# Optimization experiments

Hardware: AMD Instinct MI355X
Metric: run time of the kernel (lower is better)

The kernel has to match this reference:

```python
import jax, jax.numpy as jnp
import numpy as np

NUM_GRAPHS = 256
NEG_SLOPE = 0.2


def gat_layer(x, src, dst, W, a_src, a_dst, bias, concat):
    # x: [N, Fin], W: [Fin, H*C], a_src/a_dst: [H, C], bias: [H*C] or [C]
    N = x.shape[0]
    H, C = a_src.shape
    xl = (x @ W).reshape(N, H, C)                      # per-head projections
    e_src = jnp.sum(xl * a_src, axis=-1)               # [N, H]
    e_dst = jnp.sum(xl * a_dst, axis=-1)               # [N, H]
    e = jax.nn.leaky_relu(e_src[src] + e_dst[dst], NEG_SLOPE)  # [E, H]
    # edge softmax over variable-size neighbor sets (grouped by dst)
    m = jax.ops.segment_max(e, dst, num_segments=N)    # [N, H]
    m = jnp.where(jnp.isfinite(m), m, 0.0)
    ee = jnp.exp(e - m[dst])
    s = jax.ops.segment_sum(ee, dst, num_segments=N)   # [N, H]
    alpha = ee / (s[dst] + 1e-16)                      # [E, H]
    msg = alpha[:, :, None] * xl[src]                  # [E, H, C]
    out = jax.ops.segment_sum(msg, dst, num_segments=N)  # [N, H, C]
    out = out.reshape(N, H * C) if concat else out.mean(axis=1)
    return out + bias


def setup_inputs() -> dict:
    key = jax.random.key(0)
    ks = jax.random.split(key, 12)
    N, E, Fin, H, C, Fout = 100000, 1600000, 128, 8, 16, 64
    x = jax.random.normal(ks[0], (N, Fin), dtype=jnp.float32)
    edge_index = jax.random.randint(ks[1], (2, E), 0, N, dtype=jnp.int32)
    batch = jnp.sort(jax.random.randint(ks[2], (N,), 0, NUM_GRAPHS, dtype=jnp.int32))
    sc = 0.1
    W1 = jax.random.normal(ks[3], (Fin, H * C), dtype=jnp.float32) * sc
    att_src1 = jax.random.normal(ks[4], (H, C), dtype=jnp.float32) * sc
    att_dst1 = jax.random.normal(ks[5], (H, C), dtype=jnp.float32) * sc
    bias1 = jnp.zeros((H * C,), dtype=jnp.float32)
    W2 = jax.random.normal(ks[6], (H * C, Fout), dtype=jnp.float32) * sc
    att_src2 = jax.random.normal(ks[7], (1, Fout), dtype=jnp.float32) * sc
    att_dst2 = jax.random.normal(ks[8], (1, Fout), dtype=jnp.float32) * sc
    bias2 = jnp.zeros((Fout,), dtype=jnp.float32)
    return {"x": x, "W1": W1, "att_src1": att_src1, "att_dst1": att_dst1,
            "bias1": bias1, "W2": W2, "att_src2": att_src2, "att_dst2": att_dst2,
            "bias2": bias2, "edge_index": edge_index, "batch": batch}


def reference(x, W1, att_src1, att_dst1, bias1, W2, att_src2, att_dst2, bias2,
              edge_index, batch):
    N = x.shape[0]
    loop = jnp.arange(N, dtype=edge_index.dtype)
    src = jnp.concatenate([edge_index[0], loop])  # add self-loops (PyG default)
    dst = jnp.concatenate([edge_index[1], loop])
    # dropout is identity in eval mode
    h = gat_layer(x, src, dst, W1, att_src1, att_dst1, bias1, concat=True)
    h = jax.nn.elu(h)
    h = gat_layer(h, src, dst, W2, att_src2, att_dst2, bias2, concat=False)
    # global mean pooling over graphs
    sums = jax.ops.segment_sum(h, batch, num_segments=NUM_GRAPHS)
    cnts = jax.ops.segment_sum(jnp.ones((N,), h.dtype), batch, num_segments=NUM_GRAPHS)
    return sums / jnp.maximum(cnts, 1.0)[:, None]
```

## Files before the change

kernel.cpp:

```cpp
#include <hip/hip_runtime.h>
#include <hip/hip_fp16.h>


#define LRELU_SLOPE 0.2f
#define NBLKB 512
#define NBUCK 256
#define LOG2E 1.4426950408889634f

__device__ __forceinline__ float lrelu(float x) { return x > 0.f ? x : LRELU_SLOPE * x; }

typedef _Float16 f16x8 __attribute__((ext_vector_type(8)));
typedef float f32x4 __attribute__((ext_vector_type(4)));

__global__ __launch_bounds__(1024) void hist_conv(const int* __restrict__ ei, int E,
    int* __restrict__ bh, const float* __restrict__ W1, const float* __restrict__ W2,
    __half* __restrict__ Wt1, __half* __restrict__ Wt2) {
  const int t = threadIdx.x;
  if (blockIdx.x < NBLKB) {
    __shared__ int hist[NBUCK];
    if (t < NBUCK) hist[t] = 0;
    __syncthreads();
    const int chunk = (E + NBLKB - 1) / NBLKB;
    const int s0 = blockIdx.x * chunk;
    const int s1 = min(E, s0 + chunk);
    for (int e = s0 + t; e < s1; e += 1024) atomicAdd(&hist[ei[E + e] >> 9], 1);
    __syncthreads();
    if (t < NBUCK) bh[t * NBLKB + blockIdx.x] = hist[t];
  } else {
    const int i = (blockIdx.x - NBLKB) * 1024 + t;
    if (i < 128 * 128) {
      const int k = i >> 7, m = i & 127;
      Wt1[m * 128 + k] = __float2half(W1[i]);
    } else if (i < 128 * 128 + 128 * 64) {
      const int j = i - 128 * 128;
      const int k = j >> 6, m = j & 63;
      Wt2[m * 128 + k] = __float2half(W2[j]);
    }
  }
}

__global__ __launch_bounds__(256) void scanA(int* __restrict__ a, int* __restrict__ ctot, int N) {
  __shared__ int sm[256];
  const int base = blockIdx.x * 1024;
  const int t = threadIdx.x;
  int v[4], s = 0;
#pragma unroll
  for (int i = 0; i < 4; ++i) {
    const int idx = base + t * 4 + i;
    v[i] = (idx < N) ? a[idx] : 0;
    s += v[i];
  }
  sm[t] = s;
  __syncthreads();
  for (int o = 1; o < 256; o <<= 1) {
    const int x = (t >= o) ? sm[t - o] : 0;
    __syncthreads();
    sm[t] += x;
    __syncthreads();
  }
  if (t == 255) ctot[blockIdx.x] = sm[255];
  int run = sm[t] - s;
#pragma unroll
  for (int i = 0; i < 4; ++i) {
    const int idx = base + t * 4 + i;
    if (idx < N) a[idx] = run;
    run += v[i];
  }
}

__global__ __launch_bounds__(256) void scanC(int* __restrict__ a,
    const int* __restrict__ ctot, int NCH, int Ntot) {
  __shared__ int sc[128];
  const int t = threadIdx.x;
  if (t < 128) sc[t] = (t < NCH) ? ctot[t] : 0;
  __syncthreads();
  for (int o = 1; o < 128; o <<= 1) {
    int x = 0;
    if (t < 128 && t >= o) x = sc[t - o];
    __syncthreads();
    if (t < 128) sc[t] += x;
    __syncthreads();
  }
  const int i = blockIdx.x * 256 + t;
  if (i < Ntot) {
    const int c = i >> 10;
    a[i] += (c == 0) ? 0 : sc[c - 1];
  }
}

__global__ __launch_bounds__(1024) void bucket_scatter(const int* __restrict__ ei, int E,
    const int* __restrict__ bh, int* __restrict__ eb) {
  __shared__ int offs[NBUCK];
  const int t = threadIdx.x;
  if (t < NBUCK) offs[t] = bh[t * NBLKB + blockIdx.x];
  __syncthreads();
  const int chunk = (E + NBLKB - 1) / NBLKB;
  const int s0 = blockIdx.x * chunk;
  const int s1 = min(E, s0 + chunk);
  for (int e = s0 + t; e < s1; e += 1024) {
    const int s = ei[e], d = ei[E + e];
    const int pos = atomicAdd(&offs[d >> 9], 1);
    eb[pos] = (s << 9) | (d & 511);
  }
}

__global__ __launch_bounds__(512) void csrb_gemm1(
    const int* __restrict__ eb, const int* __restrict__ bh, int E,
    int* __restrict__ rowptr, int* __restrict__ csr, int nbCsr,
    const float* __restrict__ X, const __half* __restrict__ Wt,
    __half* __restrict__ Y, const float* __restrict__ as,
    const float* __restrict__ ad, float* __restrict__ es, float* __restrict__ ed,
    int N) {
  __shared__ union U {
    struct { int deg[512]; int sm[512]; } c;
    _Float16 xl[128 * 136];
  } u;
  const int t = threadIdx.x;

  if (blockIdx.x < nbCsr) {
    const int bucket = blockIdx.x;
    const int bstart = bh[bucket * NBLKB];
    const int bend = (bucket + 1 < NBUCK) ? bh[(bucket + 1) * NBLKB] : E;
    const int n0 = bucket << 9;
    u.c.deg[t] = 0;
    __syncthreads();
    for (int j = bstart + t; j < bend; j += 512) atomicAdd(&u.c.deg[eb[j] & 511], 1);
    __syncthreads();
    const int v = u.c.deg[t];
    u.c.sm[t] = v;
    __syncthreads();
    for (int o = 1; o < 512; o <<= 1) {
      const int x = (t >= o) ? u.c.sm[t - o] : 0;
      __syncthreads();
      u.c.sm[t] += x;
      __syncthreads();
    }
    if (n0 + t < N) rowptr[n0 + t] = bstart + u.c.sm[t];
    u.c.deg[t] = bstart + u.c.sm[t] - v;
    __syncthreads();
    for (int j = bstart + t; j < bend; j += 512) {
      const int e = eb[j];
      const int pos = atomicAdd(&u.c.deg[e & 511], 1);
      csr[pos] = e >> 9;
    }
  } else {
    constexpr int K = 128, LP = 136, NT = 8;
    const int row0 = (blockIdx.x - nbCsr) * 128;
    for (int i = t; i < 128 * (K / 4); i += 512) {
      const int r = i / (K / 4), c4 = (i % (K / 4)) * 4;
      int gr = row0 + r; if (gr >= N) gr = N - 1;
      const float4 vv = *(const float4*)(X + (size_t)gr * K + c4);
      _Float16* d = &u.xl[r * LP + c4];
      d[0] = (_Float16)vv.x; d[1] = (_Float16)vv.y;
      d[2] = (_Float16)vv.z; d[3] = (_Float16)vv.w;
    }
    __syncthreads();

    const int w = t >> 6, l = t & 63;
    const int lrow = l & 15, lk = (l >> 4) * 8;
    f32x4 acc[NT];
#pragma unroll
    for (int n = 0; n < NT; ++n) acc[n] = (f32x4){0.f, 0.f, 0.f, 0.f};
#pragma unroll
    for (int kk = 0; kk < K; kk += 32) {
      const f16x8 a = *(const f16x8*)&u.xl[(w * 16 + lrow) * LP + kk + lk];
#pragma unroll
      for (int n = 0; n < NT; ++n) {
        const f16x8 b = *(const f16x8*)((const _Float16*)Wt +
                          (size_t)(n * 16 + lrow) * K + kk + lk);
        acc[n] = __builtin_amdgcn_mfma_f32_16x16x32_f16(a, b, acc[n], 0, 0, 0);
      }
    }
    const int orow = row0 + w * 16 + (l >> 4) * 4;
#pragma unroll
    for (int n = 0; n < NT; ++n) {
#pragma unroll
      for (int j = 0; j < 4; ++j) {
        const int gr = orow + j;
        if (gr < N) Y[(size_t)gr * 128 + n * 16 + lrow] = __float2half(acc[n][j]);
      }
    }
#pragma unroll
    for (int n = 0; n < NT; ++n) {
#pragma unroll
      for (int j = 0; j < 4; ++j) {
        float ps = acc[n][j] * as[n * 16 + lrow];
        float pd = acc[n][j] * ad[n * 16 + lrow];
#pragma unroll
        for (int o = 1; o <= 8; o <<= 1) {
          ps += __shfl_xor(ps, o);
          pd += __shfl_xor(pd, o);
        }
        if (lrow == n) {
          const int gr = orow + j;
          if (gr < N) { es[gr * 8 + n] = ps * LOG2E; ed[gr * 8 + n] = pd * LOG2E; }
        }
      }
    }
  }
}

__global__ __launch_bounds__(512) void gemm2(const __half* __restrict__ X,
    const __half* __restrict__ Wt, __half* __restrict__ Y,
    const float* __restrict__ as, const float* __restrict__ ad,
    float* __restrict__ es, float* __restrict__ ed, int N) {
  constexpr int K = 128, BM = 128, LP = 136, NT = 4;
  __shared__ _Float16 Xl[BM * LP];
  const int tid = threadIdx.x;
  const int row0 = blockIdx.x * BM;
  for (int i = tid; i < BM * (K / 8); i += 512) {
    const int r = i / (K / 8), c8 = (i % (K / 8)) * 8;
    int gr = row0 + r; if (gr >= N) gr = N - 1;
    const f16x8 v = *(const f16x8*)((const _Float16*)X + (size_t)gr * K + c8);
    *(f16x8*)&Xl[r * LP + c8] = v;
  }
  __syncthreads();
  const int w = tid >> 6, l = tid & 63;
  const int lrow = l & 15, lk = (l >> 4) * 8;
  f32x4 acc[NT];
#pragma unroll
  for (int n = 0; n < NT; ++n) acc[n] = (f32x4){0.f, 0.f, 0.f, 0.f};
#pragma unroll
  for (int kk = 0; kk < K; kk += 32) {
    const f16x8 a = *(const f16x8*)&Xl[(w * 16 + lrow) * LP + kk + lk];
#pragma unroll
    for (int n = 0; n < NT; ++n) {
      const f16x8 b = *(const f16x8*)((const _Float16*)Wt +
                        (size_t)(n * 16 + lrow) * K + kk + lk);
      acc[n] = __builtin_amdgcn_mfma_f32_16x16x32_f16(a, b, acc[n], 0, 0, 0);
    }
  }
  const int orow = row0 + w * 16 + (l >> 4) * 4;
#pragma unroll
  for (int n = 0; n < NT; ++n) {
#pragma unroll
    for (int j = 0; j < 4; ++j) {
      const int gr = orow + j;
      if (gr < N) Y[(size_t)gr * 64 + n * 16 + lrow] = __float2half(acc[n][j]);
    }
  }
#pragma unroll
  for (int j = 0; j < 4; ++j) {
    float ps = 0.f, pd = 0.f;
#pragma unroll
    for (int n = 0; n < NT; ++n) {
      ps += acc[n][j] * as[n * 16 + lrow];
      pd += acc[n][j] * ad[n * 16 + lrow];
    }
#pragma unroll
    for (int o = 1; o <= 8; o <<= 1) {
      ps += __shfl_xor(ps, o);
      pd += __shfl_xor(pd, o);
    }
    if (lrow == 0) {
      const int gr = orow + j;
      if (gr < N) { es[gr] = ps * LOG2E; ed[gr] = pd * LOG2E; }
    }
  }
}

__global__ __launch_bounds__(256) void gather_h8(const __half* __restrict__ xl,
    const float* __restrict__ es, const float* __restrict__ ed,
    const int* __restrict__ rowptr, const int* __restrict__ csr,
    const float* __restrict__ bias, __half* __restrict__ hout, int N) {
  const int wave = threadIdx.x >> 6, lane = threadIdx.x & 63;
  const int n = blockIdx.x * 4 + wave;
  if (n >= N) return;
  const int sub = lane >> 4;
  const int sl  = lane & 15;
  const int c0  = sl * 8;
  const int h   = sl >> 1;
  const float edv = ed[n * 8 + h];
  const int start = (n == 0) ? 0 : rowptr[n - 1];
  const int end   = rowptr[n];
  union U16 { uint4 u; __half2 h2[4]; };

  float acc[8] = {0.f, 0.f, 0.f, 0.f, 0.f, 0.f, 0.f, 0.f};
  float ssum = 0.f;
  if (sub == 0) {
    const float ee = exp2f(lrelu(es[n * 8 + h] + edv));
    U16 r; r.u = *(const uint4*)&xl[(size_t)n * 128 + c0];
#pragma unroll
    for (int q = 0; q < 4; ++q) {
      acc[2 * q]     = fmaf(ee, __low2float(r.h2[q]),  acc[2 * q]);
      acc[2 * q + 1] = fmaf(ee, __high2float(r.h2[q]), acc[2 * q + 1]);
    }
    ssum = ee;
  }
  int j = start + sub;
  for (; j + 4 < end; j += 8) {
    const int s0 = csr[j], s1 = csr[j + 4];
    const float e0 = es[s0 * 8 + h], e1 = es[s1 * 8 + h];
    U16 r0, r1;
    r0.u = *(const uint4*)&xl[(size_t)s0 * 128 + c0];
    r1.u = *(const uint4*)&xl[(size_t)s1 * 128 + c0];
    const float ee0 = exp2f(lrelu(e0 + edv));
    const float ee1 = exp2f(lrelu(e1 + edv));
#pragma unroll
    for (int q = 0; q < 4; ++q) {
      acc[2 * q]     = fmaf(ee0, __low2float(r0.h2[q]),  acc[2 * q]);
      acc[2 * q]     = fmaf(ee1, __low2float(r1.h2[q]),  acc[2 * q]);
      acc[2 * q + 1] = fmaf(ee0, __high2float(r0.h2[q]), acc[2 * q + 1]);
      acc[2 * q + 1] = fmaf(ee1, __high2float(r1.h2[q]), acc[2 * q + 1]);
    }
    ssum += ee0 + ee1;
  }
  for (; j < end; j += 4) {
    const int src = csr[j];
    const float ee = exp2f(lrelu(es[src * 8 + h] + edv));
    U16 r; r.u = *(const uint4*)&xl[(size_t)src * 128 + c0];
#pragma unroll
    for (int q = 0; q < 4; ++q) {
      acc[2 * q]     = fmaf(ee, __low2float(r.h2[q]),  acc[2 * q]);
      acc[2 * q + 1] = fmaf(ee, __high2float(r.h2[q]), acc[2 * q + 1]);
    }
    ssum += ee;
  }
#pragma unroll
  for (int o = 16; o <= 32; o <<= 1) {
#pragma unroll
    for (int q = 0; q < 8; ++q) acc[q] += __shfl_xor(acc[q], o);
    ssum += __shfl_xor(ssum, o);
  }
  if (sub == 0) {
    const float inv = 1.f / (ssum + 1e-16f);
    const float4 b0 = *(const float4*)&bias[c0];
    const float4 b1 = *(const float4*)&bias[c0 + 4];
    float v[8];
    v[0] = acc[0] * inv + b0.x; v[1] = acc[1] * inv + b0.y;
    v[2] = acc[2] * inv + b0.z; v[3] = acc[3] * inv + b0.w;
    v[4] = acc[4] * inv + b1.x; v[5] = acc[5] * inv + b1.y;
    v[6] = acc[6] * inv + b1.z; v[7] = acc[7] * inv + b1.w;
#pragma unroll
    for (int q = 0; q < 8; ++q) v[q] = v[q] > 0.f ? v[q] : __expf(v[q]) - 1.f;
    U16 o;
#pragma unroll
    for (int q = 0; q < 4; ++q) o.h2[q] = __floats2half2_rn(v[2 * q], v[2 * q + 1]);
    *(uint4*)&hout[(size_t)n * 128 + c0] = o.u;
  }
}

__global__ __launch_bounds__(256) void gather_h1(const __half* __restrict__ xl2,
    const float* __restrict__ es, const float* __restrict__ ed,
    const int* __restrict__ rowptr, const int* __restrict__ csr,
    const float* __restrict__ bias, float* __restrict__ vout, int N) {
  const int wave = threadIdx.x >> 6, lane = threadIdx.x & 63;
  const int n = blockIdx.x * 4 + wave;
  if (n >= N) return;
  const int sub = lane >> 3;
  const int sl  = lane & 7;
  const int c0  = sl * 8;
  const float edv = ed[n];
  const int start = (n == 0) ? 0 : rowptr[n - 1];
  const int end   = rowptr[n];
  union U16 { uint4 u; __half2 h2[4]; };

  float acc[8] = {0.f, 0.f, 0.f, 0.f, 0.f, 0.f, 0.f, 0.f};
  float ssum = 0.f;
  if (sub == 0) {
    const float ee = exp2f(lrelu(es[n] + edv));
    U16 r; r.u = *(const uint4*)&xl2[(size_t)n * 64 + c0];
#pragma unroll
    for (int q = 0; q < 4; ++q) {
      acc[2 * q]     = fmaf(ee, __low2float(r.h2[q]),  acc[2 * q]);
      acc[2 * q + 1] = fmaf(ee, __high2float(r.h2[q]), acc[2 * q + 1]);
    }
    ssum = ee;
  }
  int j = start + sub;
  for (; j + 8 < end; j += 16) {
    const int s0 = csr[j], s1 = csr[j + 8];
    const float e0 = es[s0], e1 = es[s1];
    U16 r0, r1;
    r0.u = *(const uint4*)&xl2[(size_t)s0 * 64 + c0];
    r1.u = *(const uint4*)&xl2[(size_t)s1 * 64 + c0];
    const float ee0 = exp2f(lrelu(e0 + edv));
    const float ee1 = exp2f(lrelu(e1 + edv));
#pragma unroll
    for (int q = 0; q < 4; ++q) {
      acc[2 * q]     = fmaf(ee0, __low2float(r0.h2[q]),  acc[2 * q]);
      acc[2 * q]     = fmaf(ee1, __low2float(r1.h2[q]),  acc[2 * q]);
      acc[2 * q + 1] = fmaf(ee0, __high2float(r0.h2[q]), acc[2 * q + 1]);
      acc[2 * q + 1] = fmaf(ee1, __high2float(r1.h2[q]), acc[2 * q + 1]);
    }
    ssum += ee0 + ee1;
  }
  for (; j < end; j += 8) {
    const int src = csr[j];
    const float ee = exp2f(lrelu(es[src] + edv));
    U16 r; r.u = *(const uint4*)&xl2[(size_t)src * 64 + c0];
#pragma unroll
    for (int q = 0; q < 4; ++q) {
      acc[2 * q]     = fmaf(ee, __low2float(r.h2[q]),  acc[2 * q]);
      acc[2 * q + 1] = fmaf(ee, __high2float(r.h2[q]), acc[2 * q + 1]);
    }
    ssum += ee;
  }
#pragma unroll
  for (int o = 8; o <= 32; o <<= 1) {
#pragma unroll
    for (int q = 0; q < 8; ++q) acc[q] += __shfl_xor(acc[q], o);
    ssum += __shfl_xor(ssum, o);
  }
  if (sub == 0) {
    const float inv = 1.f / (ssum + 1e-16f);
    const float4 b0 = *(const float4*)&bias[c0];
    const float4 b1 = *(const float4*)&bias[c0 + 4];
    float4 o0, o1;
    o0.x = acc[0] * inv + b0.x; o0.y = acc[1] * inv + b0.y;
    o0.z = acc[2] * inv + b0.z; o0.w = acc[3] * inv + b0.w;
    o1.x = acc[4] * inv + b1.x; o1.y = acc[5] * inv + b1.y;
    o1.z = acc[6] * inv + b1.z; o1.w = acc[7] * inv + b1.w;
    *(float4*)&vout[(size_t)n * 64 + c0] = o0;
    *(float4*)&vout[(size_t)n * 64 + c0 + 4] = o1;
  }
}

__global__ __launch_bounds__(256) void pool_seg(const float* __restrict__ v,
    const int* __restrict__ batch, float* __restrict__ out, int N) {
  const int g = blockIdx.x;
  const int t = threadIdx.x;
  int lo = 0, hi = N;
  while (lo < hi) { const int m = (lo + hi) >> 1; if (batch[m] < g) lo = m + 1; else hi = m; }
  const int start = lo;
  hi = N;
  while (lo < hi) { const int m = (lo + hi) >> 1; if (batch[m] <= g) lo = m + 1; else hi = m; }
  const int end = lo;

  const int c = t & 63, rg = t >> 6;
  float s = 0.f;
  for (int r = start + rg; r < end; r += 4) s += v[(size_t)r * 64 + c];
  __shared__ float sm[256];
  sm[t] = s;
  __syncthreads();
  if (t < 64) {
    const float tot = sm[t] + sm[t + 64] + sm[t + 128] + sm[t + 192];
    out[g * 64 + t] = tot / fmaxf((float)(end - start), 1.f);
  }
}

extern "C" void kernel_launch(void* const* d_in, const int* in_sizes, int n_in,
                              void* d_out, int out_size, void* d_ws, size_t ws_size,
                              hipStream_t stream) {
  const float* x   = (const float*)d_in[0];
  const float* W1  = (const float*)d_in[1];
  const float* as1 = (const float*)d_in[2];
  const float* ad1 = (const float*)d_in[3];
  const float* b1  = (const float*)d_in[4];
  const float* W2  = (const float*)d_in[5];
  const float* as2 = (const float*)d_in[6];
  const float* ad2 = (const float*)d_in[7];
  const float* b2  = (const float*)d_in[8];
  const int* ei    = (const int*)d_in[9];
  const int* batch = (const int*)d_in[10];
  float* out = (float*)d_out;
  const int N = in_sizes[10];
  const int E = in_sizes[9] / 2;
  const int G = out_size / 64;
  const int BH = NBUCK * NBLKB;
  const int nbCsr = (N + 511) / 512;
  const int nbGemm1 = (N + 127) / 128;

  char* ws = (char*)d_ws;
  __half* xl  = (__half*)ws;
  __half* h   = (__half*)(ws + (size_t)N * 256);
  __half* xl2 = xl;
  float* vbuf = (float*)(ws + (size_t)N * 256);
  float* es1  = (float*)(ws + (size_t)N * 512);
  float* ed1  = es1 + (size_t)N * 8;
  float* es2  = es1;
  float* ed2  = es1 + N;
  int* rowptr = (int*)(ed1 + (size_t)N * 8);
  int* csr    = rowptr + N;
  int* eb     = csr + E;
  int* bh     = eb + E;
  int* ctot   = bh + BH;
  __half* Wt1 = (__half*)((((uintptr_t)(ctot + 128)) + 31) & ~(uintptr_t)31);
  __half* Wt2 = Wt1 + 128 * 128;

  hist_conv<<<NBLKB + 24, 1024, 0, stream>>>(ei, E, bh, W1, W2, Wt1, Wt2);
  scanA<<<BH / 1024, 256, 0, stream>>>(bh, ctot, BH);
  scanC<<<BH / 256, 256, 0, stream>>>(bh, ctot, BH / 1024, BH);
  bucket_scatter<<<NBLKB, 1024, 0, stream>>>(ei, E, bh, eb);

  csrb_gemm1<<<nbCsr + nbGemm1, 512, 0, stream>>>(eb, bh, E, rowptr, csr, nbCsr,
      x, Wt1, xl, as1, ad1, es1, ed1, N);
  gather_h8<<<(N + 3) / 4, 256, 0, stream>>>(xl, es1, ed1, rowptr, csr, b1, h, N);

  gemm2<<<(N + 127) / 128, 512, 0, stream>>>(h, Wt2, xl2, as2, ad2, es2, ed2, N);
  gather_h1<<<(N + 3) / 4, 256, 0, stream>>>(xl2, es2, ed2, rowptr, csr, b2, vbuf, N);

  pool_seg<<<G, 256, 0, stream>>>(vbuf, batch, out, N);
}
```

Measured before the change: 266.6 us.

## Split layer-1 GEMM across bucket-scatter and CSR-build kernels for overlap

Moves the layer-1 GEMM body into a shared device function and runs part of its row tiles (5/8) inside the bucket-scatter kernel and the rest inside the CSR-build kernel. The memory- and atomic-bound scatter and CSR-build work then runs alongside compute-bound MFMA work in the same launches, which should balance the two. The histogram and scatter kernels also drop from 1024- to 512-thread blocks, and the weight conversion now uses two looping blocks instead of 24. The fixed 5/8 split may leave one kernel longer than the other, and the larger GEMM shared buffer in the scatter kernel could lower its occupancy.

Result: slower. 291.2 us (+9.3%).

```diff
diff --git a/kernel.cpp b/kernel.cpp
--- a/kernel.cpp
+++ b/kernel.cpp
@@ -12,7 +12,67 @@
 typedef _Float16 f16x8 __attribute__((ext_vector_type(8)));
 typedef float f32x4 __attribute__((ext_vector_type(4)));
 
-__global__ __launch_bounds__(1024) void hist_conv(const int* __restrict__ ei, int E,
+__device__ __forceinline__ void gemm1_block(int gb, int t,
+    const float* __restrict__ X, const __half* __restrict__ Wt,
+    __half* __restrict__ Y, const float* __restrict__ as,
+    const float* __restrict__ ad, float* __restrict__ es, float* __restrict__ ed,
+    int N, _Float16* xl ) {
+  constexpr int K = 128, LP = 136, NT = 8;
+  const int row0 = gb * 128;
+  for (int i = t; i < 128 * (K / 4); i += 512) {
+    const int r = i / (K / 4), c4 = (i % (K / 4)) * 4;
+    int gr = row0 + r; if (gr >= N) gr = N - 1;
+    const float4 vv = *(const float4*)(X + (size_t)gr * K + c4);
+    _Float16* d = &xl[r * LP + c4];
+    d[0] = (_Float16)vv.x; d[1] = (_Float16)vv.y;
+    d[2] = (_Float16)vv.z; d[3] = (_Float16)vv.w;
+  }
+  __syncthreads();
+
+  const int w = t >> 6, l = t & 63;
+  const int lrow = l & 15, lk = (l >> 4) * 8;
+  f32x4 acc[NT];
+#pragma unroll
+  for (int n = 0; n < NT; ++n) acc[n] = (f32x4){0.f, 0.f, 0.f, 0.f};
+#pragma unroll
+  for (int kk = 0; kk < K; kk += 32) {
+    const f16x8 a = *(const f16x8*)&xl[(w * 16 + lrow) * LP + kk + lk];
+#pragma unroll
+    for (int n = 0; n < NT; ++n) {
+      const f16x8 b = *(const f16x8*)((const _Float16*)Wt +
+                        (size_t)(n * 16 + lrow) * K + kk + lk);
+      acc[n] = __builtin_amdgcn_mfma_f32_16x16x32_f16(a, b, acc[n], 0, 0, 0);
+    }
+  }
+  const int orow = row0 + w * 16 + (l >> 4) * 4;
+#pragma unroll
+  for (int n = 0; n < NT; ++n) {
+#pragma unroll
+    for (int j = 0; j < 4; ++j) {
+      const int gr = orow + j;
+      if (gr < N) Y[(size_t)gr * 128 + n * 16 + lrow] = __float2half(acc[n][j]);
+    }
+  }
+#pragma unroll
+  for (int n = 0; n < NT; ++n) {
+#pragma unroll
+    for (int j = 0; j < 4; ++j) {
+      float ps = acc[n][j] * as[n * 16 + lrow];
+      float pd = acc[n][j] * ad[n * 16 + lrow];
+#pragma unroll
+      for (int o = 1; o <= 8; o <<= 1) {
+        ps += __shfl_xor(ps, o);
+        pd += __shfl_xor(pd, o);
+      }
+      if (lrow == n) {
+        const int gr = orow + j;
+        if (gr < N) { es[gr * 8 + n] = ps * LOG2E; ed[gr * 8 + n] = pd * LOG2E; }
+      }
+    }
+  }
+}
+
+__global__ __launch_bounds__(512) void hist_conv(const int* __restrict__ ei, int E,
     int* __restrict__ bh, const float* __restrict__ W1, const float* __restrict__ W2,
     __half* __restrict__ Wt1, __half* __restrict__ Wt2) {
   const int t = threadIdx.x;
@@ -23,18 +83,18 @@
     const int chunk = (E + NBLKB - 1) / NBLKB;
     const int s0 = blockIdx.x * chunk;
     const int s1 = min(E, s0 + chunk);
-    for (int e = s0 + t; e < s1; e += 1024) atomicAdd(&hist[ei[E + e] >> 9], 1);
+    for (int e = s0 + t; e < s1; e += 512) atomicAdd(&hist[ei[E + e] >> 9], 1);
     __syncthreads();
     if (t < NBUCK) bh[t * NBLKB + blockIdx.x] = hist[t];
-  } else {
-    const int i = (blockIdx.x - NBLKB) * 1024 + t;
-    if (i < 128 * 128) {
+  } else if (blockIdx.x == NBLKB) {
+    for (int i = t; i < 128 * 128; i += 512) {
       const int k = i >> 7, m = i & 127;
       Wt1[m * 128 + k] = __float2half(W1[i]);
-    } else if (i < 128 * 128 + 128 * 64) {
-      const int j = i - 128 * 128;
-      const int k = j >> 6, m = j & 63;
-      Wt2[m * 128 + k] = __float2half(W2[j]);
+    }
+  } else {
+    for (int i = t; i < 128 * 64; i += 512) {
+      const int k = i >> 6, m = i & 63;
+      Wt2[m * 128 + k] = __float2half(W2[i]);
     }
   }
 }
@@ -88,25 +148,33 @@
   }
 }
 
-__global__ __launch_bounds__(1024) void bucket_scatter(const int* __restrict__ ei, int E,
-    const int* __restrict__ bh, int* __restrict__ eb) {
-  __shared__ int offs[NBUCK];
+__global__ __launch_bounds__(512) void scatter_gemm(const int* __restrict__ ei, int E,
+    const int* __restrict__ bh, int* __restrict__ eb,
+    const float* __restrict__ X, const __half* __restrict__ Wt,
+    __half* __restrict__ Y, const float* __restrict__ as,
+    const float* __restrict__ ad, float* __restrict__ es, float* __restrict__ ed,
+    int N) {
+  __shared__ union U { int offs[NBUCK]; _Float16 xl[128 * 136]; } u;
   const int t = threadIdx.x;
-  if (t < NBUCK) offs[t] = bh[t * NBLKB + blockIdx.x];
-  __syncthreads();
-  const int chunk = (E + NBLKB - 1) / NBLKB;
-  const int s0 = blockIdx.x * chunk;
-  const int s1 = min(E, s0 + chunk);
-  for (int e = s0 + t; e < s1; e += 1024) {
-    const int s = ei[e], d = ei[E + e];
-    const int pos = atomicAdd(&offs[d >> 9], 1);
-    eb[pos] = (s << 9) | (d & 511);
-  }
-}
-
-__global__ __launch_bounds__(512) void csrb_gemm1(
+  if (blockIdx.x < NBLKB) {
+    if (t < NBUCK) u.offs[t] = bh[t * NBLKB + blockIdx.x];
+    __syncthreads();
+    const int chunk = (E + NBLKB - 1) / NBLKB;
+    const int s0 = blockIdx.x * chunk;
+    const int s1 = min(E, s0 + chunk);
+    for (int e = s0 + t; e < s1; e += 512) {
+      const int s = ei[e], d = ei[E + e];
+      const int pos = atomicAdd(&u.offs[d >> 9], 1);
+      eb[pos] = (s << 9) | (d & 511);
+    }
+  } else {
+    gemm1_block(blockIdx.x - NBLKB, t, X, Wt, Y, as, ad, es, ed, N, u.xl);
+  }
+}
+
+__global__ __launch_bounds__(512) void csrb_gemm(
     const int* __restrict__ eb, const int* __restrict__ bh, int E,
-    int* __restrict__ rowptr, int* __restrict__ csr, int nbCsr,
+    int* __restrict__ rowptr, int* __restrict__ csr, int nbCsr, int gOff,
     const float* __restrict__ X, const __half* __restrict__ Wt,
     __half* __restrict__ Y, const float* __restrict__ as,
     const float* __restrict__ ad, float* __restrict__ es, float* __restrict__ ed,
@@ -144,59 +212,7 @@
       csr[pos] = e >> 9;
     }
   } else {
-    constexpr int K = 128, LP = 136, NT = 8;
-    const int row0 = (blockIdx.x - nbCsr) * 128;
-    for (int i = t; i < 128 * (K / 4); i += 512) {
-      const int r = i / (K / 4), c4 = (i % (K / 4)) * 4;
-      int gr = row0 + r; if (gr >= N) gr = N - 1;
-      const float4 vv = *(const float4*)(X + (size_t)gr * K + c4);
-      _Float16* d = &u.xl[r * LP + c4];
-      d[0] = (_Float16)vv.x; d[1] = (_Float16)vv.y;
-      d[2] = (_Float16)vv.z; d[3] = (_Float16)vv.w;
-    }
-    __syncthreads();
-
-    const int w = t >> 6, l = t & 63;
-    const int lrow = l & 15, lk = (l >> 4) * 8;
-    f32x4 acc[NT];
-#pragma unroll
-    for (int n = 0; n < NT; ++n) acc[n] = (f32x4){0.f, 0.f, 0.f, 0.f};
-#pragma unroll
-    for (int kk = 0; kk < K; kk += 32) {
-      const f16x8 a = *(const f16x8*)&u.xl[(w * 16 + lrow) * LP + kk + lk];
-#pragma unroll
-      for (int n = 0; n < NT; ++n) {
-        const f16x8 b = *(const f16x8*)((const _Float16*)Wt +
-                          (size_t)(n * 16 + lrow) * K + kk + lk);
-        acc[n] = __builtin_amdgcn_mfma_f32_16x16x32_f16(a, b, acc[n], 0, 0, 0);
-      }
-    }
-    const int orow = row0 + w * 16 + (l >> 4) * 4;
-#pragma unroll
-    for (int n = 0; n < NT; ++n) {
-#pragma unroll
-      for (int j = 0; j < 4; ++j) {
-        const int gr = orow + j;
-        if (gr < N) Y[(size_t)gr * 128 + n * 16 + lrow] = __float2half(acc[n][j]);
-      }
-    }
-#pragma unroll
-    for (int n = 0; n < NT; ++n) {
-#pragma unroll
-      for (int j = 0; j < 4; ++j) {
-        float ps = acc[n][j] * as[n * 16 + lrow];
-        float pd = acc[n][j] * ad[n * 16 + lrow];
-#pragma unroll
-        for (int o = 1; o <= 8; o <<= 1) {
-          ps += __shfl_xor(ps, o);
-          pd += __shfl_xor(pd, o);
-        }
-        if (lrow == n) {
-          const int gr = orow + j;
-          if (gr < N) { es[gr * 8 + n] = ps * LOG2E; ed[gr * 8 + n] = pd * LOG2E; }
-        }
-      }
-    }
+    gemm1_block(gOff + blockIdx.x - nbCsr, t, X, Wt, Y, as, ad, es, ed, N, u.xl);
   }
 }
 
@@ -460,6 +476,8 @@
   const int BH = NBUCK * NBLKB;
   const int nbCsr = (N + 511) / 512;
   const int nbGemm1 = (N + 127) / 128;
+  const int GA = (nbGemm1 * 5) / 8;
+  const int GB = nbGemm1 - GA;
 
   char* ws = (char*)d_ws;
   __half* xl  = (__half*)ws;
@@ -478,13 +496,14 @@
   __half* Wt1 = (__half*)((((uintptr_t)(ctot + 128)) + 31) & ~(uintptr_t)31);
   __half* Wt2 = Wt1 + 128 * 128;
 
-  hist_conv<<<NBLKB + 24, 1024, 0, stream>>>(ei, E, bh, W1, W2, Wt1, Wt2);
+  hist_conv<<<NBLKB + 2, 512, 0, stream>>>(ei, E, bh, W1, W2, Wt1, Wt2);
   scanA<<<BH / 1024, 256, 0, stream>>>(bh, ctot, BH);
   scanC<<<BH / 256, 256, 0, stream>>>(bh, ctot, BH / 1024, BH);
-  bucket_scatter<<<NBLKB, 1024, 0, stream>>>(ei, E, bh, eb);
-
-  csrb_gemm1<<<nbCsr + nbGemm1, 512, 0, stream>>>(eb, bh, E, rowptr, csr, nbCsr,
+  scatter_gemm<<<NBLKB + GA, 512, 0, stream>>>(ei, E, bh, eb,
       x, Wt1, xl, as1, ad1, es1, ed1, N);
+  csrb_gemm<<<nbCsr + GB, 512, 0, stream>>>(eb, bh, E, rowptr, csr, nbCsr, GA,
+      x, Wt1, xl, as1, ad1, es1, ed1, N);
+
   gather_h8<<<(N + 3) / 4, 256, 0, stream>>>(xl, es1, ed1, rowptr, csr, b1, h, N);
 
   gemm2<<<(N + 127) / 128, 512, 0, stream>>>(h, Wt2, xl2, as2, ad2, es2, ed2, N);
```
